# Kernel tuning notes

Measured on AMD Instinct MI355X. Metric: run time of the kernel, lower is better.

Reference implementation:

```python
import jax, jax.numpy as jnp
import numpy as np

TOP_K = 6
NORM_TOPK_PROB = True


def setup_inputs() -> dict:
    key = jax.random.key(0)
    k1, k2 = jax.random.split(key)
    hidden_states = jax.random.normal(k1, (4, 4096, 2048), dtype=jnp.float32)
    # kaiming_uniform_(a=sqrt(5)) on (E, H): bound = sqrt(6/((1+5)*H)) = 1/sqrt(H)
    bound = 1.0 / np.sqrt(2048)
    weight = jax.random.uniform(k2, (64, 2048), dtype=jnp.float32, minval=-bound, maxval=bound)
    return {"hidden_states": hidden_states, "weight": weight}


def reference(hidden_states, weight):
    bsz, seq_len, h = hidden_states.shape
    x = hidden_states.reshape(-1, h)                      # [T, H]
    logits = jnp.einsum("th,eh->te", x, weight)           # [T, E]
    topk_weight, topk_idx = jax.lax.top_k(logits, TOP_K)  # [T, K]
    topk_weight = jax.nn.softmax(topk_weight, axis=-1)
    if TOP_K > 1 and NORM_TOPK_PROB:
        denom = jnp.sum(topk_weight, axis=-1, keepdims=True) + 1e-20
        topk_weight = topk_weight / denom
    # eval path: aux_loss is None; return routing indices and weights
    return topk_idx, topk_weight
```

## Files before the change

### kernel.cpp

```cpp
#include <hip/hip_runtime.h>
#include <math.h>

#define NTOK 16384
#define HDIM 2048
#define NEXP 64
#define TOPK 6
#define TB   32
#define CH   64
#define NCH  (HDIM / CH)
#define XPAD 68

union SMem {
    struct {
        float ws[NEXP][CH];
        float xs[TB][XPAD];
    } s;
    struct {
        float4 h1[2][16][16][4];
        float  lg[TB][NEXP + 1];
    } e;
};

#define FMA4(A, X, W)                      \
    A.x = fmaf(X.x, W.x, A.x);             \
    A.y = fmaf(X.y, W.y, A.y);             \
    A.z = fmaf(X.z, W.z, A.z);             \
    A.w = fmaf(X.w, W.w, A.w);

__global__ __launch_bounds__(256, 2) void moe_gate_kernel(
        const float* __restrict__ x,
        const float* __restrict__ w,
        float* __restrict__ out)
{
    __shared__ SMem sm;

    const int tid   = threadIdx.x;
    const int wv    = tid >> 6;
    const int lane  = tid & 63;
    const int hh    = wv >> 1;
    const int ts    = wv & 1;
    const int q     = lane >> 4;
    const int eg    = lane & 15;
    const int tbase = blockIdx.x * TB;
    const int tokL  = 16 * ts + 4 * q;

    float4 acc[4][4];
    #pragma unroll
    for (int r = 0; r < 4; ++r)
        #pragma unroll
        for (int s = 0; s < 4; ++s)
            acc[r][s] = make_float4(0.f, 0.f, 0.f, 0.f);

    for (int ck = 0; ck < NCH; ++ck) {
        #pragma unroll
        for (int k = 0; k < 2; ++k) {
            const int f = tid + 256 * k;
            const int row = f >> 4, slot = f & 15;
            *(float4*)&sm.s.xs[row][4 * slot] =
                *(const float4*)&x[(size_t)(tbase + row) * HDIM + ck * CH + 4 * slot];
        }
        #pragma unroll
        for (int k = 0; k < 4; ++k) {
            const int f = tid + 256 * k;
            const int row = f >> 4, slot = f & 15;
            *(float4*)&sm.s.ws[row][4 * (slot ^ ((row >> 2) & 7))] =
                *(const float4*)&w[(size_t)row * HDIM + ck * CH + 4 * slot];
        }
        __syncthreads();

        {
            const float* xb = &sm.s.xs[tokL][0];
            const char*  wb = (const char*)&sm.s.ws[4 * eg][0];
            const int    kx = (eg & 7) << 4;
            #pragma unroll
            for (int st = 0; st < 8; ++st) {
                const int slot  = 8 * hh + st;
                const int sbyte = (slot << 4) ^ kx;
                const float4 w0 = *(const float4*)(wb + sbyte);
                const float4 w1 = *(const float4*)(wb + sbyte + CH * 4);
                const float4 w2 = *(const float4*)(wb + sbyte + CH * 8);
                const float4 w3 = *(const float4*)(wb + sbyte + CH * 12);
                const float4 x0 = *(const float4*)(xb + 4 * slot);
                const float4 x1 = *(const float4*)(xb + XPAD + 4 * slot);
                const float4 x2 = *(const float4*)(xb + 2 * XPAD + 4 * slot);
                const float4 x3 = *(const float4*)(xb + 3 * XPAD + 4 * slot);
                FMA4(acc[0][0], x0, w0) FMA4(acc[0][1], x0, w1)
                FMA4(acc[0][2], x0, w2) FMA4(acc[0][3], x0, w3)
                FMA4(acc[1][0], x1, w0) FMA4(acc[1][1], x1, w1)
                FMA4(acc[1][2], x1, w2) FMA4(acc[1][3], x1, w3)
                FMA4(acc[2][0], x2, w0) FMA4(acc[2][1], x2, w1)
                FMA4(acc[2][2], x2, w2) FMA4(acc[2][3], x2, w3)
                FMA4(acc[3][0], x3, w0) FMA4(acc[3][1], x3, w1)
                FMA4(acc[3][2], x3, w2) FMA4(acc[3][3], x3, w3)
            }
        }
        __syncthreads();
    }

    if (hh == 1) {
        #pragma unroll
        for (int r = 0; r < 4; ++r)
            #pragma unroll
            for (int s = 0; s < 4; ++s)
                sm.e.h1[ts][4 * q + r][eg][s] = acc[r][s];
    }
    __syncthreads();
    if (hh == 0) {
        #pragma unroll
        for (int r = 0; r < 4; ++r)
            #pragma unroll
            for (int s = 0; s < 4; ++s) {
                const float4 o  = sm.e.h1[ts][4 * q + r][eg][s];
                const float  J0 = acc[r][s].x + o.x;
                const float  J1 = acc[r][s].y + o.y;
                const float  J2 = acc[r][s].z + o.z;
                const float  J3 = acc[r][s].w + o.w;
                sm.e.lg[tokL + r][4 * eg + s] = (J0 + J2) + (J1 + J3);
            }
    }
    __syncthreads();

    if (tid < TB) {
        float val[TOPK];
        int   idx[TOPK];
        #pragma unroll
        for (int k = 0; k < TOPK; ++k) { val[k] = -3.0e38f; idx[k] = 0; }

        for (int e = 0; e < NEXP; ++e) {
            float cv = sm.e.lg[tid][e];
            int   ci = e;
            #pragma unroll
            for (int k = 0; k < TOPK; ++k) {
                if (cv > val[k]) {
                    const float tv = val[k]; const int ti = idx[k];
                    val[k] = cv; idx[k] = ci;
                    cv = tv; ci = ti;
                }
            }
        }

        const float m = val[0];
        float ex[TOPK];
        float s = 0.f;
        #pragma unroll
        for (int k = 0; k < TOPK; ++k) { ex[k] = expf(val[k] - m); s += ex[k]; }
        float p[TOPK];
        float d = 0.f;
        #pragma unroll
        for (int k = 0; k < TOPK; ++k) { p[k] = ex[k] / s; d += p[k]; }
        d += 1e-20f;

        const int tg = tbase + tid;
        float* oi = out;
        float* ow = out + (size_t)NTOK * TOPK;
        #pragma unroll
        for (int k = 0; k < TOPK; ++k) {
            oi[tg * TOPK + k] = (float)idx[k];
            ow[tg * TOPK + k] = p[k] / d;
        }
    }
}

extern "C" void kernel_launch(void* const* d_in, const int* in_sizes, int n_in,
                              void* d_out, int out_size, void* d_ws, size_t ws_size,
                              hipStream_t stream) {
    const float* x = (const float*)d_in[0];
    const float* w = (const float*)d_in[1];
    float* out = (float*)d_out;
    dim3 grid(NTOK / TB);
    dim3 block(256);
    hipLaunchKernelGGL(moe_gate_kernel, grid, block, 0, stream, x, w, out);
}
```

Before: 117.3 us.

## Stream x from global into registers and double-buffer weights via direct-to-LDS loads

```diff
diff --git a/kernel.cpp b/kernel.cpp
--- a/kernel.cpp
+++ b/kernel.cpp
@@ -5,21 +5,24 @@
 #define HDIM 2048
 #define NEXP 64
 #define TOPK 6
-#define TB   32
+#define TB   16
 #define CH   64
 #define NCH  (HDIM / CH)
-#define XPAD 68
+#define CHB  256
 
 union SMem {
+    float ws[2][NEXP][CH];
     struct {
-        float ws[NEXP][CH];
-        float xs[TB][XPAD];
-    } s;
-    struct {
-        float4 h1[2][16][16][4];
+        float4 cmb[TB][16][4];
         float  lg[TB][NEXP + 1];
     } e;
 };
+
+__device__ __forceinline__ void gload_lds16(const float* g, void* l) {
+    __builtin_amdgcn_global_load_lds(
+        (const __attribute__((address_space(1))) unsigned int*)g,
+        (__attribute__((address_space(3))) unsigned int*)l, 16, 0, 0);
+}
 
 #define FMA4(A, X, W)                      \
     A.x = fmaf(X.x, W.x, A.x);             \
@@ -27,7 +30,24 @@
     A.z = fmaf(X.z, W.z, A.z);             \
     A.w = fmaf(X.w, W.w, A.w);
 
-__global__ __launch_bounds__(256, 2) void moe_gate_kernel(
+#define STEP(XV, ST)                                                        \
+    {                                                                       \
+        const int sbyte = (((8 * hh + (ST)) << 4)) ^ kx;                    \
+        const float4 w0 = *(const float4*)(wb + sbyte);                     \
+        const float4 w1 = *(const float4*)(wb + sbyte + CH * 4);            \
+        const float4 w2 = *(const float4*)(wb + sbyte + CH * 8);            \
+        const float4 w3 = *(const float4*)(wb + sbyte + CH * 12);           \
+        FMA4(acc[0][0], XV[0], w0) FMA4(acc[0][1], XV[0], w1)               \
+        FMA4(acc[0][2], XV[0], w2) FMA4(acc[0][3], XV[0], w3)               \
+        FMA4(acc[1][0], XV[1], w0) FMA4(acc[1][1], XV[1], w1)               \
+        FMA4(acc[1][2], XV[1], w2) FMA4(acc[1][3], XV[1], w3)               \
+        FMA4(acc[2][0], XV[2], w0) FMA4(acc[2][1], XV[2], w1)               \
+        FMA4(acc[2][2], XV[2], w2) FMA4(acc[2][3], XV[2], w3)               \
+        FMA4(acc[3][0], XV[3], w0) FMA4(acc[3][1], XV[3], w1)               \
+        FMA4(acc[3][2], XV[3], w2) FMA4(acc[3][3], XV[3], w3)               \
+    }
+
+__global__ __launch_bounds__(128) void moe_gate_kernel(
         const float* __restrict__ x,
         const float* __restrict__ w,
         float* __restrict__ out)
@@ -35,14 +55,17 @@
     __shared__ SMem sm;
 
     const int tid   = threadIdx.x;
-    const int wv    = tid >> 6;
     const int lane  = tid & 63;
-    const int hh    = wv >> 1;
-    const int ts    = wv & 1;
+    const int hh    = tid >> 6;
     const int q     = lane >> 4;
     const int eg    = lane & 15;
+    const int kx    = (eg & 7) << 4;
     const int tbase = blockIdx.x * TB;
-    const int tokL  = 16 * ts + 4 * q;
+
+    const char* xq[4];
+    #pragma unroll
+    for (int r = 0; r < 4; ++r)
+        xq[r] = (const char*)(x + (size_t)(tbase + 4 * q + r) * HDIM) + 128 * hh;
 
     float4 acc[4][4];
     #pragma unroll
@@ -51,50 +74,63 @@
         for (int s = 0; s < 4; ++s)
             acc[r][s] = make_float4(0.f, 0.f, 0.f, 0.f);
 
-    for (int ck = 0; ck < NCH; ++ck) {
-        #pragma unroll
-        for (int k = 0; k < 2; ++k) {
-            const int f = tid + 256 * k;
-            const int row = f >> 4, slot = f & 15;
-            *(float4*)&sm.s.xs[row][4 * slot] =
-                *(const float4*)&x[(size_t)(tbase + row) * HDIM + ck * CH + 4 * slot];
-        }
-        #pragma unroll
-        for (int k = 0; k < 4; ++k) {
-            const int f = tid + 256 * k;
-            const int row = f >> 4, slot = f & 15;
-            *(float4*)&sm.s.ws[row][4 * (slot ^ ((row >> 2) & 7))] =
-                *(const float4*)&w[(size_t)row * HDIM + ck * CH + 4 * slot];
-        }
+    float4 xA[4], xB[4];
+
+    #pragma unroll
+    for (int k = 0; k < 8; ++k) {
+        const int i0 = 128 * k + 64 * hh;
+        const int i  = i0 + lane;
+        const int e  = i >> 4;
+        const int gs = (i & 15) ^ ((e >> 2) & 7);
+        gload_lds16(w + (size_t)e * HDIM + 4 * gs,
+                    (char*)&sm.ws[0][0][0] + 16 * (size_t)i0);
+    }
+    #pragma unroll
+    for (int r = 0; r < 4; ++r)
+        xA[r] = *(const float4*)(xq[r]);
+    __syncthreads();
+
+    for (int c = 0; c < NCH; ++c) {
+        const int buf = c & 1;
+        const char* wb = (const char*)&sm.ws[buf][4 * eg][0];
+
+        #pragma unroll
+        for (int r = 0; r < 4; ++r)
+            xB[r] = *(const float4*)(xq[r] + 16);
+
+        if (c + 1 < NCH) {
+            #pragma unroll
+            for (int k = 0; k < 8; ++k) {
+                const int i0 = 128 * k + 64 * hh;
+                const int i  = i0 + lane;
+                const int e  = i >> 4;
+                const int gs = (i & 15) ^ ((e >> 2) & 7);
+                gload_lds16(w + (size_t)e * HDIM + (size_t)(c + 1) * CH + 4 * gs,
+                            (char*)&sm.ws[buf ^ 1][0][0] + 16 * (size_t)i0);
+            }
+        }
+
+        STEP(xA, 0)
+
+        #pragma unroll
+        for (int st = 1; st < 8; ++st) {
+            if (st < 7) {
+                float4* dst = ((st + 1) & 1) ? xB : xA;
+                #pragma unroll
+                for (int r = 0; r < 4; ++r)
+                    dst[r] = *(const float4*)(xq[r] + 16 * (st + 1));
+            } else if (c + 1 < NCH) {
+                #pragma unroll
+                for (int r = 0; r < 4; ++r)
+                    xA[r] = *(const float4*)(xq[r] + CHB);
+            }
+            if (st & 1) STEP(xB, st) else STEP(xA, st)
+        }
+
+        #pragma unroll
+        for (int r = 0; r < 4; ++r)
+            xq[r] += CHB;
         __syncthreads();
-
-        {
-            const float* xb = &sm.s.xs[tokL][0];
-            const char*  wb = (const char*)&sm.s.ws[4 * eg][0];
-            const int    kx = (eg & 7) << 4;
-            #pragma unroll
-            for (int st = 0; st < 8; ++st) {
-                const int slot  = 8 * hh + st;
-                const int sbyte = (slot << 4) ^ kx;
-                const float4 w0 = *(const float4*)(wb + sbyte);
-                const float4 w1 = *(const float4*)(wb + sbyte + CH * 4);
-                const float4 w2 = *(const float4*)(wb + sbyte + CH * 8);
-                const float4 w3 = *(const float4*)(wb + sbyte + CH * 12);
-                const float4 x0 = *(const float4*)(xb + 4 * slot);
-                const float4 x1 = *(const float4*)(xb + XPAD + 4 * slot);
-                const float4 x2 = *(const float4*)(xb + 2 * XPAD + 4 * slot);
-                const float4 x3 = *(const float4*)(xb + 3 * XPAD + 4 * slot);
-                FMA4(acc[0][0], x0, w0) FMA4(acc[0][1], x0, w1)
-                FMA4(acc[0][2], x0, w2) FMA4(acc[0][3], x0, w3)
-                FMA4(acc[1][0], x1, w0) FMA4(acc[1][1], x1, w1)
-                FMA4(acc[1][2], x1, w2) FMA4(acc[1][3], x1, w3)
-                FMA4(acc[2][0], x2, w0) FMA4(acc[2][1], x2, w1)
-                FMA4(acc[2][2], x2, w2) FMA4(acc[2][3], x2, w3)
-                FMA4(acc[3][0], x3, w0) FMA4(acc[3][1], x3, w1)
-                FMA4(acc[3][2], x3, w2) FMA4(acc[3][3], x3, w3)
-            }
-        }
-        __syncthreads();
     }
 
     if (hh == 1) {
@@ -102,7 +138,7 @@
         for (int r = 0; r < 4; ++r)
             #pragma unroll
             for (int s = 0; s < 4; ++s)
-                sm.e.h1[ts][4 * q + r][eg][s] = acc[r][s];
+                sm.e.cmb[4 * q + r][eg][s] = acc[r][s];
     }
     __syncthreads();
     if (hh == 0) {
@@ -110,12 +146,12 @@
         for (int r = 0; r < 4; ++r)
             #pragma unroll
             for (int s = 0; s < 4; ++s) {
-                const float4 o  = sm.e.h1[ts][4 * q + r][eg][s];
+                const float4 o  = sm.e.cmb[4 * q + r][eg][s];
                 const float  J0 = acc[r][s].x + o.x;
                 const float  J1 = acc[r][s].y + o.y;
                 const float  J2 = acc[r][s].z + o.z;
                 const float  J3 = acc[r][s].w + o.w;
-                sm.e.lg[tokL + r][4 * eg + s] = (J0 + J2) + (J1 + J3);
+                sm.e.lg[4 * q + r][4 * eg + s] = (J0 + J2) + (J1 + J3);
             }
     }
     __syncthreads();
@@ -168,6 +204,6 @@
     const float* w = (const float*)d_in[1];
     float* out = (float*)d_out;
     dim3 grid(NTOK / TB);
-    dim3 block(256);
+    dim3 block(128);
     hipLaunchKernelGGL(moe_gate_kernel, grid, block, 0, stream, x, w, out);
 }
```

Measured after the change: 207.3 us. +76.7%, slower.

## Double-buffer LDS chunks using direct global-to-LDS async loads

Applied to the files above, without the earlier changes.

```diff
diff --git a/kernel.cpp b/kernel.cpp
--- a/kernel.cpp
+++ b/kernel.cpp
@@ -8,24 +8,74 @@
 #define TB   32
 #define CH   64
 #define NCH  (HDIM / CH)
-#define XPAD 68
 
 union SMem {
     struct {
-        float ws[NEXP][CH];
-        float xs[TB][XPAD];
+        float ws[2][NEXP][CH];
+        float xs[2][TB][CH];
     } s;
     struct {
-        float4 h1[2][16][16][4];
+        float4 cmb[2][16][16][4];
         float  lg[TB][NEXP + 1];
     } e;
 };
+
+__device__ __forceinline__ void gload_lds16(const float* g, void* l) {
+    __builtin_amdgcn_global_load_lds(
+        (const __attribute__((address_space(1))) unsigned int*)g,
+        (__attribute__((address_space(3))) unsigned int*)l, 16, 0, 0);
+}
+
+__device__ __forceinline__ void stage_chunk(const float* __restrict__ x,
+                                            const float* __restrict__ w,
+                                            float* wsb, float* xsb,
+                                            int tbase, int c, int wv, int lane) {
+    #pragma unroll
+    for (int k = 0; k < 4; ++k) {
+        const int i0 = 64 * (4 * wv + k);
+        const int i  = i0 + lane;
+        const int e  = i >> 4;
+        const int sl = (i & 15) ^ ((e >> 2) & 7);
+        gload_lds16(w + (size_t)e * HDIM + (size_t)c * CH + 4 * sl, wsb + 4 * i0);
+    }
+    #pragma unroll
+    for (int k = 0; k < 2; ++k) {
+        const int i0 = 64 * (2 * wv + k);
+        const int i  = i0 + lane;
+        const int t  = i >> 4;
+        const int sl = (i & 15) ^ ((t >> 2) & 3);
+        gload_lds16(x + (size_t)(tbase + t) * HDIM + (size_t)c * CH + 4 * sl, xsb + 4 * i0);
+    }
+}
 
 #define FMA4(A, X, W)                      \
     A.x = fmaf(X.x, W.x, A.x);             \
     A.y = fmaf(X.y, W.y, A.y);             \
     A.z = fmaf(X.z, W.z, A.z);             \
     A.w = fmaf(X.w, W.w, A.w);
+
+#define STEP(ST)                                                            \
+    {                                                                       \
+        const int so = ((8 * hh + (ST)) << 4);                              \
+        const int wo = so ^ kx;                                             \
+        const int xo = so ^ kq;                                             \
+        const float4 w0 = *(const float4*)(wb + wo);                        \
+        const float4 w1 = *(const float4*)(wb + wo + CH * 4);               \
+        const float4 w2 = *(const float4*)(wb + wo + CH * 8);               \
+        const float4 w3 = *(const float4*)(wb + wo + CH * 12);              \
+        const float4 x0 = *(const float4*)(xb0 + xo);                       \
+        const float4 x1 = *(const float4*)(xb0 + 256 + xo);                 \
+        const float4 x2 = *(const float4*)(xb0 + 512 + xo);                 \
+        const float4 x3 = *(const float4*)(xb0 + 768 + xo);                 \
+        FMA4(acc[0][0], x0, w0) FMA4(acc[0][1], x0, w1)                     \
+        FMA4(acc[0][2], x0, w2) FMA4(acc[0][3], x0, w3)                     \
+        FMA4(acc[1][0], x1, w0) FMA4(acc[1][1], x1, w1)                     \
+        FMA4(acc[1][2], x1, w2) FMA4(acc[1][3], x1, w3)                     \
+        FMA4(acc[2][0], x2, w0) FMA4(acc[2][1], x2, w1)                     \
+        FMA4(acc[2][2], x2, w2) FMA4(acc[2][3], x2, w3)                     \
+        FMA4(acc[3][0], x3, w0) FMA4(acc[3][1], x3, w1)                     \
+        FMA4(acc[3][2], x3, w2) FMA4(acc[3][3], x3, w3)                     \
+    }
 
 __global__ __launch_bounds__(256, 2) void moe_gate_kernel(
         const float* __restrict__ x,
@@ -41,6 +91,8 @@
     const int ts    = wv & 1;
     const int q     = lane >> 4;
     const int eg    = lane & 15;
+    const int kx    = (eg & 7) << 4;
+    const int kq    = q << 4;
     const int tbase = blockIdx.x * TB;
     const int tokL  = 16 * ts + 4 * q;
 
@@ -51,49 +103,20 @@
         for (int s = 0; s < 4; ++s)
             acc[r][s] = make_float4(0.f, 0.f, 0.f, 0.f);
 
-    for (int ck = 0; ck < NCH; ++ck) {
-        #pragma unroll
-        for (int k = 0; k < 2; ++k) {
-            const int f = tid + 256 * k;
-            const int row = f >> 4, slot = f & 15;
-            *(float4*)&sm.s.xs[row][4 * slot] =
-                *(const float4*)&x[(size_t)(tbase + row) * HDIM + ck * CH + 4 * slot];
-        }
-        #pragma unroll
-        for (int k = 0; k < 4; ++k) {
-            const int f = tid + 256 * k;
-            const int row = f >> 4, slot = f & 15;
-            *(float4*)&sm.s.ws[row][4 * (slot ^ ((row >> 2) & 7))] =
-                *(const float4*)&w[(size_t)row * HDIM + ck * CH + 4 * slot];
-        }
-        __syncthreads();
+    stage_chunk(x, w, &sm.s.ws[0][0][0], &sm.s.xs[0][0][0], tbase, 0, wv, lane);
+    __syncthreads();
 
-        {
-            const float* xb = &sm.s.xs[tokL][0];
-            const char*  wb = (const char*)&sm.s.ws[4 * eg][0];
-            const int    kx = (eg & 7) << 4;
-            #pragma unroll
-            for (int st = 0; st < 8; ++st) {
-                const int slot  = 8 * hh + st;
-                const int sbyte = (slot << 4) ^ kx;
-                const float4 w0 = *(const float4*)(wb + sbyte);
-                const float4 w1 = *(const float4*)(wb + sbyte + CH * 4);
-                const float4 w2 = *(const float4*)(wb + sbyte + CH * 8);
-                const float4 w3 = *(const float4*)(wb + sbyte + CH * 12);
-                const float4 x0 = *(const float4*)(xb + 4 * slot);
-                const float4 x1 = *(const float4*)(xb + XPAD + 4 * slot);
-                const float4 x2 = *(const float4*)(xb + 2 * XPAD + 4 * slot);
-                const float4 x3 = *(const float4*)(xb + 3 * XPAD + 4 * slot);
-                FMA4(acc[0][0], x0, w0) FMA4(acc[0][1], x0, w1)
-                FMA4(acc[0][2], x0, w2) FMA4(acc[0][3], x0, w3)
-                FMA4(acc[1][0], x1, w0) FMA4(acc[1][1], x1, w1)
-                FMA4(acc[1][2], x1, w2) FMA4(acc[1][3], x1, w3)
-                FMA4(acc[2][0], x2, w0) FMA4(acc[2][1], x2, w1)
-                FMA4(acc[2][2], x2, w2) FMA4(acc[2][3], x2, w3)
-                FMA4(acc[3][0], x3, w0) FMA4(acc[3][1], x3, w1)
-                FMA4(acc[3][2], x3, w2) FMA4(acc[3][3], x3, w3)
-            }
-        }
+    for (int c = 0; c < NCH; ++c) {
+        const int buf = c & 1;
+
+        if (c + 1 < NCH)
+            stage_chunk(x, w, &sm.s.ws[buf ^ 1][0][0], &sm.s.xs[buf ^ 1][0][0],
+                        tbase, c + 1, wv, lane);
+
+        const char* wb  = (const char*)&sm.s.ws[buf][4 * eg][0];
+        const char* xb0 = (const char*)&sm.s.xs[buf][tokL][0];
+        STEP(0) STEP(1) STEP(2) STEP(3) STEP(4) STEP(5) STEP(6) STEP(7)
+
         __syncthreads();
     }
 
@@ -102,7 +125,7 @@
         for (int r = 0; r < 4; ++r)
             #pragma unroll
             for (int s = 0; s < 4; ++s)
-                sm.e.h1[ts][4 * q + r][eg][s] = acc[r][s];
+                sm.e.cmb[ts][4 * q + r][eg][s] = acc[r][s];
     }
     __syncthreads();
     if (hh == 0) {
@@ -110,7 +133,7 @@
         for (int r = 0; r < 4; ++r)
             #pragma unroll
             for (int s = 0; s < 4; ++s) {
-                const float4 o  = sm.e.h1[ts][4 * q + r][eg][s];
+                const float4 o  = sm.e.cmb[ts][4 * q + r][eg][s];
                 const float  J0 = acc[r][s].x + o.x;
                 const float  J1 = acc[r][s].y + o.y;
                 const float  J2 = acc[r][s].z + o.z;
```

Result: slower. 157.0 us (+33.8%).
